# Kernel tuning notes

Hardware: AMD Instinct MI355X
Metric: run time of the kernel (lower is better)

## Reference

```python
import jax, jax.numpy as jnp
import numpy as np

N_NODES = 50000
NFEAT = 512
NHID = 128
N_EDGES = 800000
LN_EPS = 1e-5


def setup_inputs() -> dict:
    key = jax.random.key(0)
    k1, k2, k3, k4, k5 = jax.random.split(key, 5)
    h = jax.random.normal(k1, (N_NODES, NFEAT), dtype=jnp.float32)
    src = jax.random.randint(k2, (N_EDGES,), 0, N_NODES, dtype=jnp.int32)
    dst = jax.random.randint(k3, (N_EDGES,), 0, N_NODES, dtype=jnp.int32)
    # GraphConv params (glorot-ish) + bias; LayerNorm affine params
    W = jax.random.normal(k4, (NFEAT, NHID), dtype=jnp.float32) / np.sqrt(NFEAT)
    b = jnp.zeros((NHID,), dtype=jnp.float32)
    gamma = jnp.ones((NHID,), dtype=jnp.float32)
    beta = jnp.zeros((NHID,), dtype=jnp.float32)
    return {"h": h, "src": src, "dst": dst, "W": W, "b": b, "gamma": gamma, "beta": beta}


def reference(h, src, dst, W, b, gamma, beta):
    n = h.shape[0]
    ones = jnp.ones_like(src, dtype=jnp.float32)
    out_deg = jax.ops.segment_sum(ones, src, num_segments=n)
    in_deg = jax.ops.segment_sum(ones, dst, num_segments=n)
    out_norm = jnp.maximum(out_deg, 1.0) ** -0.5  # [N]
    in_norm = jnp.maximum(in_deg, 1.0) ** -0.5    # [N]

    # norm='both': scale source features by out_deg^{-1/2}
    x = h * out_norm[:, None]
    # in_feats > out_feats -> DGL multiplies by W before aggregation
    x = x @ W  # [N, NHID]
    # sparse aggregate: sum messages over incoming edges
    agg = jax.ops.segment_sum(x[src], dst, num_segments=n)  # [N, NHID]
    agg = agg * in_norm[:, None] + b

    # LayerNorm over last dim
    mu = jnp.mean(agg, axis=-1, keepdims=True)
    var = jnp.mean((agg - mu) ** 2, axis=-1, keepdims=True)
    y = (agg - mu) * jax.lax.rsqrt(var + LN_EPS) * gamma + beta
    return y
```

## Files before the change

### kernel.cpp

```cpp
#include <hip/hip_runtime.h>

#define N_NODES 50000
#define NFEAT   512
#define NHID    128
#define N_EDGES 800000
#define LN_EPS  1e-5f

#define GEMM_ROWS   32
#define GEMM_BLOCKS ((N_NODES + GEMM_ROWS - 1) / GEMM_ROWS)
#define DEG_BLOCKS  (N_EDGES / 256)
#define NB_SCAN     ((N_NODES + 1023) / 1024)

typedef __attribute__((ext_vector_type(8))) short bf16x8;
typedef __attribute__((ext_vector_type(4))) float fx4;

__device__ __forceinline__ unsigned short f2bf(float f) {
    union { float f; unsigned u; } v; v.f = f;
    unsigned r = v.u + 0x7FFF + ((v.u >> 16) & 1);
    return (unsigned short)(r >> 16);
}

__device__ __forceinline__ void bf2x(unsigned u, float& lo, float& hi) {
    union { unsigned u; float f; } a, b;
    a.u = u << 16;
    b.u = u & 0xFFFF0000u;
    lo = a.f; hi = b.f;
}

__global__ __launch_bounds__(256) void prep_kernel(
    const float* __restrict__ W, unsigned short* __restrict__ wf,
    int4* __restrict__ zero_ptr)
{
    int t = blockIdx.x * 256 + threadIdx.x;
#pragma unroll
    for (int i = t; i < 25088; i += 16384)
        zero_ptr[i] = make_int4(0, 0, 0, 0);

    if (blockIdx.x < 32) {
        int lane = t & 63;
        int frag = t >> 6;
        int kc = frag >> 3, tt = frag & 7;
        int n  = tt * 16 + (lane & 15);
        int k0 = kc * 32 + (lane >> 4) * 8;
        unsigned short v[8];
#pragma unroll
        for (int j = 0; j < 8; j++)
            v[j] = f2bf(W[(size_t)(k0 + j) * NHID + n]);
        *(bf16x8*)(wf + (size_t)t * 8) = *(bf16x8*)v;
    }
}

__global__ __launch_bounds__(256) void fused_gemm_degree(
    const float* __restrict__ h, const unsigned short* __restrict__ wf,
    unsigned short* __restrict__ x,
    const int* __restrict__ src, const int* __restrict__ dst,
    int* __restrict__ out_deg, int* __restrict__ in_deg,
    int* __restrict__ edge_pos)
{
    __shared__ unsigned short afrag_lds[2][16 * 64 * 8];

    const int tid = threadIdx.x;
    const int B = blockIdx.x;
    bool isDeg; int id;
    if (B < 2 * GEMM_BLOCKS) { isDeg = (B & 1); id = B >> 1; }
    else                     { isDeg = true;    id = B - GEMM_BLOCKS; }

    if (isDeg) {
        int e = id * 256 + tid;
        int s = src[e];
        int d = dst[e];
        int pos = atomicAdd(&in_deg[d], 1);
        atomicAdd(&out_deg[s], 1);
        edge_pos[e] = pos;
        return;
    }

    const int row0 = id * GEMM_ROWS;

#pragma unroll
    for (int it = 0; it < 16; it++) {
        int i = tid + it * 256;
        int r  = i >> 7;
        int grow = row0 + r;
        if (grow > N_NODES - 1) grow = N_NODES - 1;
        float4 v = ((const float4*)h)[(size_t)grow * 128 + (i & 127)];
        int g  = r >> 4;
        int rr = r & 15;
        int k0 = (i & 127) << 2;
        int kc = k0 >> 5;
        int q  = (k0 >> 3) & 3;
        int j  = k0 & 7;
        int gp = q * 16 + (rr ^ (q | ((kc & 1) << 2)));
        unsigned long long pk =
            (unsigned long long)f2bf(v.x)
          | ((unsigned long long)f2bf(v.y) << 16)
          | ((unsigned long long)f2bf(v.z) << 32)
          | ((unsigned long long)f2bf(v.w) << 48);
        *(unsigned long long*)(&afrag_lds[g][0] + kc * 512 + gp * 8 + j) = pk;
    }
    __syncthreads();

    const int wave = tid >> 6;
    const int lane = tid & 63;
    const int t0   = wave * 2;
    const int rr_l = lane & 15;
    const int q_l  = lane >> 4;
    const int g_e  = q_l * 16 + (rr_l ^ q_l);
    const int g_o  = q_l * 16 + (rr_l ^ q_l ^ 4);

    fx4 acc00 = (fx4){0.f, 0.f, 0.f, 0.f};
    fx4 acc01 = (fx4){0.f, 0.f, 0.f, 0.f};
    fx4 acc10 = (fx4){0.f, 0.f, 0.f, 0.f};
    fx4 acc11 = (fx4){0.f, 0.f, 0.f, 0.f};

    const bf16x8* a0p = (const bf16x8*)&afrag_lds[0][0];
    const bf16x8* a1p = (const bf16x8*)&afrag_lds[1][0];
    const bf16x8* wfp = (const bf16x8*)wf + t0 * 64 + lane;

#pragma unroll 4
    for (int kc = 0; kc < 16; kc++) {
        int gidx = (kc & 1) ? g_o : g_e;
        bf16x8 a0 = a0p[kc * 64 + gidx];
        bf16x8 a1 = a1p[kc * 64 + gidx];
        bf16x8 b0 = wfp[kc * 512];
        bf16x8 b1 = wfp[kc * 512 + 64];
        acc00 = __builtin_amdgcn_mfma_f32_16x16x32_bf16(a0, b0, acc00, 0, 0, 0);
        acc01 = __builtin_amdgcn_mfma_f32_16x16x32_bf16(a0, b1, acc01, 0, 0, 0);
        acc10 = __builtin_amdgcn_mfma_f32_16x16x32_bf16(a1, b0, acc10, 0, 0, 0);
        acc11 = __builtin_amdgcn_mfma_f32_16x16x32_bf16(a1, b1, acc11, 0, 0, 0);
    }

    const int q = lane >> 4;
    const int c = lane & 15;
#pragma unroll
    for (int reg = 0; reg < 4; reg++) {
        int r0 = row0 + q * 4 + reg;
        if (r0 < N_NODES) {
            unsigned short* xr = x + (size_t)r0 * NHID;
            xr[t0 * 16 + c]       = f2bf(acc00[reg]);
            xr[(t0 + 1) * 16 + c] = f2bf(acc01[reg]);
        }
        int r1 = row0 + 16 + q * 4 + reg;
        if (r1 < N_NODES) {
            unsigned short* xr = x + (size_t)r1 * NHID;
            xr[t0 * 16 + c]       = f2bf(acc10[reg]);
            xr[(t0 + 1) * 16 + c] = f2bf(acc11[reg]);
        }
    }
}

__global__ __launch_bounds__(1024) void scan_local(
    const int* __restrict__ in_deg, int* __restrict__ row_ptr, int* __restrict__ bsum,
    const int* __restrict__ out_deg, float* __restrict__ out_norm)
{
    __shared__ int wsum[16];
    const int tid = threadIdx.x;
    const int lane = tid & 63, wave = tid >> 6;
    int i = blockIdx.x * 1024 + tid;
    int v = (i < N_NODES) ? in_deg[i] : 0;
    int sv = v;
#pragma unroll
    for (int off = 1; off < 64; off <<= 1) {
        int t = __shfl_up(sv, off);
        if (lane >= off) sv += t;
    }
    if (lane == 63) wsum[wave] = sv;
    if (i < N_NODES)
        out_norm[i] = rsqrtf(fmaxf((float)out_deg[i], 1.0f));
    __syncthreads();
    if (wave == 0) {
        int wv = (lane < 16) ? wsum[lane] : 0;
#pragma unroll
        for (int off = 1; off < 16; off <<= 1) {
            int t = __shfl_up(wv, off);
            if (lane >= off) wv += t;
        }
        if (lane < 16) wsum[lane] = wv;
    }
    __syncthreads();
    int excl = ((wave > 0) ? wsum[wave - 1] : 0) + (sv - v);
    if (i < N_NODES) row_ptr[i] = excl;
    if (tid == 1023) bsum[blockIdx.x] = wsum[15];
}

__global__ __launch_bounds__(1024) void scan_add2(
    int* __restrict__ row_ptr, const int* __restrict__ bsum)
{
    __shared__ int off_s, tot_s;
    const int tid = threadIdx.x;
    if (tid < 64) {
        int v = (tid < NB_SCAN) ? bsum[tid] : 0;
        int sv = v;
#pragma unroll
        for (int off = 1; off < 64; off <<= 1) {
            int t = __shfl_up(sv, off);
            if (tid >= off) sv += t;
        }
        int pre = __shfl(sv, (blockIdx.x == 0) ? 0 : (blockIdx.x - 1));
        int tot = __shfl(sv, NB_SCAN - 1);
        if (tid == 0) {
            off_s = (blockIdx.x == 0) ? 0 : pre;
            tot_s = tot;
        }
    }
    __syncthreads();
    int i = blockIdx.x * 1024 + tid;
    if (i < N_NODES) row_ptr[i] += off_s;
    if (blockIdx.x == 0 && tid == 0) row_ptr[N_NODES] = tot_s;
}

__global__ __launch_bounds__(256) void fill_kernel(
    const int* __restrict__ src, const int* __restrict__ dst,
    const int* __restrict__ row_ptr, const int* __restrict__ edge_pos,
    int* __restrict__ csr_src)
{
    int e = blockIdx.x * 256 + threadIdx.x;
    if (e < N_EDGES) {
        int d = dst[e];
        csr_src[row_ptr[d] + edge_pos[e]] = src[e];
    }
}

__global__ __launch_bounds__(256) void aggregate_kernel(
    const unsigned short* __restrict__ x, const int* __restrict__ row_ptr,
    const int* __restrict__ csr_src, const float* __restrict__ out_norm,
    const float* __restrict__ b, const float* __restrict__ gamma,
    const float* __restrict__ beta, float* __restrict__ out)
{
    const int n    = blockIdx.x * 4 + (threadIdx.x >> 6);
    const int lane = threadIdx.x & 63;
    const int half = lane >> 5;
    const int c    = lane & 31;
    const int start = row_ptr[n];
    const int end   = row_ptr[n + 1];

    float a0 = 0.f, a1 = 0.f, a2 = 0.f, a3 = 0.f;

    for (int base = start; base < end; base += 64) {
        int me   = base + lane;
        int msrc = (me < end) ? csr_src[me] : 0;
        int cnt  = min(64, end - base);
        int npair = (cnt + 1) >> 1;
        int j = 0;
        for (; j + 4 <= npair; j += 4) {
            int i0 = 2 * j + half, i1 = i0 + 2, i2 = i0 + 4, i3 = i0 + 6;
            int s0 = __shfl(msrc, i0);
            int s1 = __shfl(msrc, i1);
            int s2 = __shfl(msrc, i2);
            int s3 = __shfl(msrc, i3);
            float w0 = (i0 < cnt) ? out_norm[s0] : 0.f;
            float w1 = (i1 < cnt) ? out_norm[s1] : 0.f;
            float w2 = (i2 < cnt) ? out_norm[s2] : 0.f;
            float w3 = (i3 < cnt) ? out_norm[s3] : 0.f;
            uint2 u0 = *(const uint2*)(x + (size_t)s0 * NHID + c * 4);
            uint2 u1 = *(const uint2*)(x + (size_t)s1 * NHID + c * 4);
            uint2 u2 = *(const uint2*)(x + (size_t)s2 * NHID + c * 4);
            uint2 u3 = *(const uint2*)(x + (size_t)s3 * NHID + c * 4);
            float p0, p1, p2, p3;
            bf2x(u0.x, p0, p1); bf2x(u0.y, p2, p3);
            a0 += p0 * w0; a1 += p1 * w0; a2 += p2 * w0; a3 += p3 * w0;
            bf2x(u1.x, p0, p1); bf2x(u1.y, p2, p3);
            a0 += p0 * w1; a1 += p1 * w1; a2 += p2 * w1; a3 += p3 * w1;
            bf2x(u2.x, p0, p1); bf2x(u2.y, p2, p3);
            a0 += p0 * w2; a1 += p1 * w2; a2 += p2 * w2; a3 += p3 * w2;
            bf2x(u3.x, p0, p1); bf2x(u3.y, p2, p3);
            a0 += p0 * w3; a1 += p1 * w3; a2 += p2 * w3; a3 += p3 * w3;
        }
        for (; j < npair; ++j) {
            int i0 = 2 * j + half;
            int s0 = __shfl(msrc, i0);
            float w0 = (i0 < cnt) ? out_norm[s0] : 0.f;
            uint2 u0 = *(const uint2*)(x + (size_t)s0 * NHID + c * 4);
            float p0, p1, p2, p3;
            bf2x(u0.x, p0, p1); bf2x(u0.y, p2, p3);
            a0 += p0 * w0; a1 += p1 * w0; a2 += p2 * w0; a3 += p3 * w0;
        }
    }

    a0 += __shfl_xor(a0, 32);
    a1 += __shfl_xor(a1, 32);
    a2 += __shfl_xor(a2, 32);
    a3 += __shfl_xor(a3, 32);

    float inorm = rsqrtf(fmaxf((float)(end - start), 1.0f));
    float4 bb = *(const float4*)(b + c * 4);
    float v0 = a0 * inorm + bb.x;
    float v1 = a1 * inorm + bb.y;
    float v2 = a2 * inorm + bb.z;
    float v3 = a3 * inorm + bb.w;

    float s = v0 + v1 + v2 + v3;
#pragma unroll
    for (int off = 16; off > 0; off >>= 1) s += __shfl_xor(s, off);
    float mu = s * (1.0f / 128.0f);

    float d0 = v0 - mu, d1 = v1 - mu, d2 = v2 - mu, d3 = v3 - mu;
    float qd = d0 * d0 + d1 * d1 + d2 * d2 + d3 * d3;
#pragma unroll
    for (int off = 16; off > 0; off >>= 1) qd += __shfl_xor(qd, off);
    float var = qd * (1.0f / 128.0f);
    float rs = rsqrtf(var + LN_EPS);

    if (half == 0) {
        float4 gg = *(const float4*)(gamma + c * 4);
        float4 be = *(const float4*)(beta + c * 4);
        float4 o;
        o.x = d0 * rs * gg.x + be.x;
        o.y = d1 * rs * gg.y + be.y;
        o.z = d2 * rs * gg.z + be.z;
        o.w = d3 * rs * gg.w + be.w;
        *(float4*)(out + (size_t)n * NHID + c * 4) = o;
    }
}

extern "C" void kernel_launch(void* const* d_in, const int* in_sizes, int n_in,
                              void* d_out, int out_size, void* d_ws, size_t ws_size,
                              hipStream_t stream) {
    const float* h     = (const float*)d_in[0];
    const int*   src   = (const int*)d_in[1];
    const int*   dst   = (const int*)d_in[2];
    const float* W     = (const float*)d_in[3];
    const float* b     = (const float*)d_in[4];
    const float* gamma = (const float*)d_in[5];
    const float* beta  = (const float*)d_in[6];
    float* out = (float*)d_out;

    char* ws = (char*)d_ws;
    const size_t DEG_BYTES = 200704;
    const size_t RP_BYTES  = 200960;
    int*            out_deg  = (int*)(ws);
    int*            in_deg   = (int*)(ws + DEG_BYTES);
    int*            row_ptr  = (int*)(ws + 2 * DEG_BYTES);
    float*          out_norm = (float*)(ws + 2 * DEG_BYTES + RP_BYTES);
    int*            bsum     = (int*)(ws + 3 * DEG_BYTES + RP_BYTES);
    int*            edge_pos = (int*)(ws + 3 * DEG_BYTES + RP_BYTES + 1024);
    int*            csr_src  = (int*)(ws + 3 * DEG_BYTES + RP_BYTES + 1024 + (size_t)N_EDGES * 4);
    unsigned short* wf       = (unsigned short*)(ws + 3 * DEG_BYTES + RP_BYTES + 1024 + 2 * (size_t)N_EDGES * 4);
    unsigned short* x        = (unsigned short*)(ws + 3 * DEG_BYTES + RP_BYTES + 1024 + 2 * (size_t)N_EDGES * 4 + 131072);

    prep_kernel<<<64, 256, 0, stream>>>(W, wf, (int4*)ws);
    fused_gemm_degree<<<GEMM_BLOCKS + DEG_BLOCKS, 256, 0, stream>>>(
        h, wf, x, src, dst, out_deg, in_deg, edge_pos);
    scan_local<<<NB_SCAN, 1024, 0, stream>>>(in_deg, row_ptr, bsum, out_deg, out_norm);
    scan_add2 <<<NB_SCAN, 1024, 0, stream>>>(row_ptr, bsum);
    fill_kernel<<<(N_EDGES + 255) / 256, 256, 0, stream>>>(src, dst, row_ptr, edge_pos, csr_src);
    aggregate_kernel<<<N_NODES / 4, 256, 0, stream>>>(
        x, row_ptr, csr_src, out_norm, b, gamma, beta, out);
}
```

Before: 254.9 us.

## Widen aggregate gathers to 16B, batch GEMM loads, stage GEMM output through LDS

```diff
diff --git a/kernel.cpp b/kernel.cpp
--- a/kernel.cpp
+++ b/kernel.cpp
@@ -57,7 +57,7 @@
     int* __restrict__ out_deg, int* __restrict__ in_deg,
     int* __restrict__ edge_pos)
 {
-    __shared__ unsigned short afrag_lds[2][16 * 64 * 8];
+    __shared__ __align__(16) unsigned short afrag_lds[2][16 * 64 * 8];
 
     const int tid = threadIdx.x;
     const int B = blockIdx.x;
@@ -78,25 +78,34 @@
     const int row0 = id * GEMM_ROWS;
 
 #pragma unroll
-    for (int it = 0; it < 16; it++) {
-        int i = tid + it * 256;
-        int r  = i >> 7;
-        int grow = row0 + r;
-        if (grow > N_NODES - 1) grow = N_NODES - 1;
-        float4 v = ((const float4*)h)[(size_t)grow * 128 + (i & 127)];
-        int g  = r >> 4;
-        int rr = r & 15;
-        int k0 = (i & 127) << 2;
-        int kc = k0 >> 5;
-        int q  = (k0 >> 3) & 3;
-        int j  = k0 & 7;
-        int gp = q * 16 + (rr ^ (q | ((kc & 1) << 2)));
-        unsigned long long pk =
-            (unsigned long long)f2bf(v.x)
-          | ((unsigned long long)f2bf(v.y) << 16)
-          | ((unsigned long long)f2bf(v.z) << 32)
-          | ((unsigned long long)f2bf(v.w) << 48);
-        *(unsigned long long*)(&afrag_lds[g][0] + kc * 512 + gp * 8 + j) = pk;
+    for (int half = 0; half < 2; half++) {
+        float4 v[8];
+#pragma unroll
+        for (int it = 0; it < 8; it++) {
+            int i = tid + (half * 8 + it) * 256;
+            int r = i >> 7;
+            int grow = row0 + r;
+            if (grow > N_NODES - 1) grow = N_NODES - 1;
+            v[it] = ((const float4*)h)[(size_t)grow * 128 + (i & 127)];
+        }
+#pragma unroll
+        for (int it = 0; it < 8; it++) {
+            int i = tid + (half * 8 + it) * 256;
+            int r  = i >> 7;
+            int g  = r >> 4;
+            int rr = r & 15;
+            int k0 = (i & 127) << 2;
+            int kc = k0 >> 5;
+            int q  = (k0 >> 3) & 3;
+            int j  = k0 & 7;
+            int gp = q * 16 + (rr ^ (q | ((kc & 1) << 2)));
+            unsigned long long pk =
+                (unsigned long long)f2bf(v[it].x)
+              | ((unsigned long long)f2bf(v[it].y) << 16)
+              | ((unsigned long long)f2bf(v[it].z) << 32)
+              | ((unsigned long long)f2bf(v[it].w) << 48);
+            *(unsigned long long*)(&afrag_lds[g][0] + kc * 512 + gp * 8 + j) = pk;
+        }
     }
     __syncthreads();
 
@@ -130,21 +139,30 @@
         acc11 = __builtin_amdgcn_mfma_f32_16x16x32_bf16(a1, b1, acc11, 0, 0, 0);
     }
 
-    const int q = lane >> 4;
-    const int c = lane & 15;
-#pragma unroll
-    for (int reg = 0; reg < 4; reg++) {
-        int r0 = row0 + q * 4 + reg;
-        if (r0 < N_NODES) {
-            unsigned short* xr = x + (size_t)r0 * NHID;
-            xr[t0 * 16 + c]       = f2bf(acc00[reg]);
-            xr[(t0 + 1) * 16 + c] = f2bf(acc01[reg]);
-        }
-        int r1 = row0 + 16 + q * 4 + reg;
-        if (r1 < N_NODES) {
-            unsigned short* xr = x + (size_t)r1 * NHID;
-            xr[t0 * 16 + c]       = f2bf(acc10[reg]);
-            xr[(t0 + 1) * 16 + c] = f2bf(acc11[reg]);
+    __syncthreads();
+    unsigned short* orow = (unsigned short*)&afrag_lds[0][0];
+    {
+        const int q = lane >> 4;
+        const int c = lane & 15;
+#pragma unroll
+        for (int reg = 0; reg < 4; reg++) {
+            int r0 = q * 4 + reg;
+            orow[r0 * 128 + t0 * 16 + c]              = f2bf(acc00[reg]);
+            orow[r0 * 128 + (t0 + 1) * 16 + c]        = f2bf(acc01[reg]);
+            orow[(16 + r0) * 128 + t0 * 16 + c]       = f2bf(acc10[reg]);
+            orow[(16 + r0) * 128 + (t0 + 1) * 16 + c] = f2bf(acc11[reg]);
+        }
+    }
+    __syncthreads();
+    {
+        const int4* osrc = (const int4*)&afrag_lds[0][0];
+#pragma unroll
+        for (int p = 0; p < 2; p++) {
+            int idx = tid + p * 256;
+            int r   = idx >> 4;
+            int gr  = row0 + r;
+            if (gr < N_NODES)
+                ((int4*)x)[(size_t)gr * 16 + (idx & 15)] = osrc[idx];
         }
     }
 }
@@ -221,6 +239,13 @@
     }
 }
 
+#define ACC4(uu, ww) {                                                    \
+    float p0,p1,p2,p3,p4,p5,p6,p7;                                        \
+    bf2x(uu.x,p0,p1); bf2x(uu.y,p2,p3);                                   \
+    bf2x(uu.z,p4,p5); bf2x(uu.w,p6,p7);                                   \
+    a0 += p0*ww; a1 += p1*ww; a2 += p2*ww; a3 += p3*ww;                   \
+    a4 += p4*ww; a5 += p5*ww; a6 += p6*ww; a7 += p7*ww; }
+
 __global__ __launch_bounds__(256) void aggregate_kernel(
     const unsigned short* __restrict__ x, const int* __restrict__ row_ptr,
     const int* __restrict__ csr_src, const float* __restrict__ out_norm,
@@ -229,87 +254,99 @@
 {
     const int n    = blockIdx.x * 4 + (threadIdx.x >> 6);
     const int lane = threadIdx.x & 63;
-    const int half = lane >> 5;
-    const int c    = lane & 31;
+    const int qi   = lane >> 4;
+    const int c    = lane & 15;
     const int start = row_ptr[n];
     const int end   = row_ptr[n + 1];
 
     float a0 = 0.f, a1 = 0.f, a2 = 0.f, a3 = 0.f;
+    float a4 = 0.f, a5 = 0.f, a6 = 0.f, a7 = 0.f;
 
     for (int base = start; base < end; base += 64) {
-        int me   = base + lane;
-        int msrc = (me < end) ? csr_src[me] : 0;
-        int cnt  = min(64, end - base);
-        int npair = (cnt + 1) >> 1;
-        int j = 0;
-        for (; j + 4 <= npair; j += 4) {
-            int i0 = 2 * j + half, i1 = i0 + 2, i2 = i0 + 4, i3 = i0 + 6;
+        int  me   = base + lane;
+        bool vld  = (me < end);
+        int  msrc = vld ? csr_src[me] : 0;
+        float mw  = vld ? out_norm[msrc] : 0.f;
+        int cnt = min(64, end - base);
+        int ng  = (cnt + 3) >> 2;
+        int g = 0;
+        for (; g + 4 <= ng; g += 4) {
+            int i0 = 4 * g + qi, i1 = i0 + 4, i2 = i0 + 8, i3 = i0 + 12;
             int s0 = __shfl(msrc, i0);
             int s1 = __shfl(msrc, i1);
             int s2 = __shfl(msrc, i2);
             int s3 = __shfl(msrc, i3);
-            float w0 = (i0 < cnt) ? out_norm[s0] : 0.f;
-            float w1 = (i1 < cnt) ? out_norm[s1] : 0.f;
-            float w2 = (i2 < cnt) ? out_norm[s2] : 0.f;
-            float w3 = (i3 < cnt) ? out_norm[s3] : 0.f;
-            uint2 u0 = *(const uint2*)(x + (size_t)s0 * NHID + c * 4);
-            uint2 u1 = *(const uint2*)(x + (size_t)s1 * NHID + c * 4);
-            uint2 u2 = *(const uint2*)(x + (size_t)s2 * NHID + c * 4);
-            uint2 u3 = *(const uint2*)(x + (size_t)s3 * NHID + c * 4);
-            float p0, p1, p2, p3;
-            bf2x(u0.x, p0, p1); bf2x(u0.y, p2, p3);
-            a0 += p0 * w0; a1 += p1 * w0; a2 += p2 * w0; a3 += p3 * w0;
-            bf2x(u1.x, p0, p1); bf2x(u1.y, p2, p3);
-            a0 += p0 * w1; a1 += p1 * w1; a2 += p2 * w1; a3 += p3 * w1;
-            bf2x(u2.x, p0, p1); bf2x(u2.y, p2, p3);
-            a0 += p0 * w2; a1 += p1 * w2; a2 += p2 * w2; a3 += p3 * w2;
-            bf2x(u3.x, p0, p1); bf2x(u3.y, p2, p3);
-            a0 += p0 * w3; a1 += p1 * w3; a2 += p2 * w3; a3 += p3 * w3;
-        }
-        for (; j < npair; ++j) {
-            int i0 = 2 * j + half;
+            float w0 = __shfl(mw, i0);
+            float w1 = __shfl(mw, i1);
+            float w2 = __shfl(mw, i2);
+            float w3 = __shfl(mw, i3);
+            uint4 u0 = *(const uint4*)(x + (size_t)s0 * NHID + c * 8);
+            uint4 u1 = *(const uint4*)(x + (size_t)s1 * NHID + c * 8);
+            uint4 u2 = *(const uint4*)(x + (size_t)s2 * NHID + c * 8);
+            uint4 u3 = *(const uint4*)(x + (size_t)s3 * NHID + c * 8);
+            ACC4(u0, w0) ACC4(u1, w1) ACC4(u2, w2) ACC4(u3, w3)
+        }
+        for (; g < ng; ++g) {
+            int i0 = 4 * g + qi;
             int s0 = __shfl(msrc, i0);
-            float w0 = (i0 < cnt) ? out_norm[s0] : 0.f;
-            uint2 u0 = *(const uint2*)(x + (size_t)s0 * NHID + c * 4);
-            float p0, p1, p2, p3;
-            bf2x(u0.x, p0, p1); bf2x(u0.y, p2, p3);
-            a0 += p0 * w0; a1 += p1 * w0; a2 += p2 * w0; a3 += p3 * w0;
-        }
-    }
-
-    a0 += __shfl_xor(a0, 32);
-    a1 += __shfl_xor(a1, 32);
-    a2 += __shfl_xor(a2, 32);
-    a3 += __shfl_xor(a3, 32);
+            float w0 = __shfl(mw, i0);
+            uint4 u0 = *(const uint4*)(x + (size_t)s0 * NHID + c * 8);
+            ACC4(u0, w0)
+        }
+    }
+
+    a0 += __shfl_xor(a0, 16); a0 += __shfl_xor(a0, 32);
+    a1 += __shfl_xor(a1, 16); a1 += __shfl_xor(a1, 32);
+    a2 += __shfl_xor(a2, 16); a2 += __shfl_xor(a2, 32);
+    a3 += __shfl_xor(a3, 16); a3 += __shfl_xor(a3, 32);
+    a4 += __shfl_xor(a4, 16); a4 += __shfl_xor(a4, 32);
+    a5 += __shfl_xor(a5, 16); a5 += __shfl_xor(a5, 32);
+    a6 += __shfl_xor(a6, 16); a6 += __shfl_xor(a6, 32);
+    a7 += __shfl_xor(a7, 16); a7 += __shfl_xor(a7, 32);
 
     float inorm = rsqrtf(fmaxf((float)(end - start), 1.0f));
-    float4 bb = *(const float4*)(b + c * 4);
-    float v0 = a0 * inorm + bb.x;
-    float v1 = a1 * inorm + bb.y;
-    float v2 = a2 * inorm + bb.z;
-    float v3 = a3 * inorm + bb.w;
-
-    float s = v0 + v1 + v2 + v3;
-#pragma unroll
-    for (int off = 16; off > 0; off >>= 1) s += __shfl_xor(s, off);
+    float4 b0 = *(const float4*)(b + c * 8);
+    float4 b1 = *(const float4*)(b + c * 8 + 4);
+    float v0 = a0 * inorm + b0.x;
+    float v1 = a1 * inorm + b0.y;
+    float v2 = a2 * inorm + b0.z;
+    float v3 = a3 * inorm + b0.w;
+    float v4 = a4 * inorm + b1.x;
+    float v5 = a5 * inorm + b1.y;
+    float v6 = a6 * inorm + b1.z;
+    float v7 = a7 * inorm + b1.w;
+
+    float s = ((v0 + v1) + (v2 + v3)) + ((v4 + v5) + (v6 + v7));
+#pragma unroll
+    for (int off = 8; off > 0; off >>= 1) s += __shfl_xor(s, off);
     float mu = s * (1.0f / 128.0f);
 
     float d0 = v0 - mu, d1 = v1 - mu, d2 = v2 - mu, d3 = v3 - mu;
-    float qd = d0 * d0 + d1 * d1 + d2 * d2 + d3 * d3;
-#pragma unroll
-    for (int off = 16; off > 0; off >>= 1) qd += __shfl_xor(qd, off);
+    float d4 = v4 - mu, d5 = v5 - mu, d6 = v6 - mu, d7 = v7 - mu;
+    float qd = ((d0*d0 + d1*d1) + (d2*d2 + d3*d3)) + ((d4*d4 + d5*d5) + (d6*d6 + d7*d7));
+#pragma unroll
+    for (int off = 8; off > 0; off >>= 1) qd += __shfl_xor(qd, off);
     float var = qd * (1.0f / 128.0f);
     float rs = rsqrtf(var + LN_EPS);
 
-    if (half == 0) {
-        float4 gg = *(const float4*)(gamma + c * 4);
-        float4 be = *(const float4*)(beta + c * 4);
+    if (lane < 16) {
+        float4 gg = *(const float4*)(gamma + c * 8);
+        float4 be = *(const float4*)(beta + c * 8);
         float4 o;
         o.x = d0 * rs * gg.x + be.x;
         o.y = d1 * rs * gg.y + be.y;
         o.z = d2 * rs * gg.z + be.z;
         o.w = d3 * rs * gg.w + be.w;
-        *(float4*)(out + (size_t)n * NHID + c * 4) = o;
+        *(float4*)(out + (size_t)n * NHID + c * 8) = o;
+    } else if (lane < 32) {
+        float4 gg = *(const float4*)(gamma + c * 8 + 4);
+        float4 be = *(const float4*)(beta + c * 8 + 4);
+        float4 o;
+        o.x = d4 * rs * gg.x + be.x;
+        o.y = d5 * rs * gg.y + be.y;
+        o.z = d6 * rs * gg.z + be.z;
+        o.w = d7 * rs * gg.w + be.w;
+        *(float4*)(out + (size_t)n * NHID + c * 8 + 4) = o;
     }
 }
 
```

Measured after the change: 253.7 us. Within noise of the previous version (-0.5%).
